# Kernel optimization log

Hardware: AMD Instinct MI355X
Metric: run time of the kernel (lower is better)

## Reference

```python
import jax, jax.numpy as jnp
import numpy as np

B, D_IN, T = 8, 1024, 2048
K, D_CB = 8192, 8
COMMIT = 0.005
CB_LOSS_W = 1.0
EPS = 1e-12  # F.normalize eps


def _wn(v, g):
    # torch weight_norm(dim=0) on a 1x1 Conv1d: w = g * v / ||v|| per output row
    return g[:, None] * v / jnp.linalg.norm(v, axis=1, keepdims=True)


def _l2n(x):
    return x / jnp.maximum(jnp.linalg.norm(x, axis=-1, keepdims=True), EPS)


def setup_inputs() -> dict:
    key = jax.random.key(0)
    ks = jax.random.split(key, 8)
    return {
        "z": jax.random.normal(ks[0], (B, D_IN, T), dtype=jnp.float32),
        "in_v": jax.random.normal(ks[1], (D_CB, D_IN), dtype=jnp.float32) * 0.02,
        "in_g": jnp.ones((D_CB,), dtype=jnp.float32),
        "in_b": jnp.zeros((D_CB,), dtype=jnp.float32),
        "out_v": jax.random.normal(ks[2], (D_IN, D_CB), dtype=jnp.float32) * 0.02,
        "out_g": jnp.ones((D_IN,), dtype=jnp.float32),
        "out_b": jnp.zeros((D_IN,), dtype=jnp.float32),
        "codebook": jax.random.normal(ks[3], (K, D_CB), dtype=jnp.float32),
    }


def reference(z, in_v, in_g, in_b, out_v, out_g, out_b, codebook):
    sg = jax.lax.stop_gradient
    # in_project: weight-normed 1x1 conv == matmul over channel dim
    w_in = _wn(in_v, in_g)
    z_e = jnp.einsum('oi,bit->bot', w_in, z) + in_b[None, :, None]  # [B, D_CB, T]

    # decode_latents
    enc = jnp.transpose(z_e, (0, 2, 1)).reshape(-1, D_CB)  # (B*T, D_CB)
    enc_n = _l2n(enc)
    cb_n = _l2n(codebook)
    dist = (jnp.sum(enc_n**2, axis=1, keepdims=True)
            - 2.0 * enc_n @ cb_n.T
            + jnp.sum(cb_n**2, axis=1)[None, :])  # (B*T, K)
    indices = jnp.argmin(dist, axis=1).reshape(B, T)  # [B, T]
    z_q = jnp.transpose(codebook[indices], (0, 2, 1))  # [B, D_CB, T] (unnormalized codebook)

    # training losses (per-batch means over (d, t))
    commit_loss = jnp.mean((z_e - sg(z_q)) ** 2, axis=(1, 2)) * COMMIT
    codebook_loss = jnp.mean((z_q - sg(z_e)) ** 2, axis=(1, 2)) * CB_LOSS_W

    # straight-through estimator
    z_q_st = z_e + sg(z_q - z_e)

    # out_project
    w_out = _wn(out_v, out_g)
    z_q_out = jnp.einsum('od,bdt->bot', w_out, z_q_st) + out_b[None, :, None]  # [B, D_IN, T]
    return (z_q_out, commit_loss, codebook_loss, indices, z_e)
```

## Files before the change

kernel.cpp:

```cpp
#include <hip/hip_runtime.h>
#include <math.h>
#include <stdint.h>

#define BB    8
#define DIN   1024
#define TT    2048
#define KK    8192
#define DCB   8
#define NPOS  (BB*TT)
#define KCHUNKS 64
#define KCH     (KK/KCHUNKS)
#define MARGIN  6e-4f

#define OFF_ZQOUT  0
#define OFF_COMMIT 16777216
#define OFF_CBLOSS 16777224
#define OFF_IDX    16777232
#define OFF_ZE     16793616

typedef short s8v __attribute__((ext_vector_type(8)));
typedef float f4v __attribute__((ext_vector_type(4)));

__device__ __forceinline__ unsigned short f2bf(float f) {
    unsigned u = __float_as_uint(f);
    u += 0x7FFF + ((u >> 16) & 1);
    return (unsigned short)(u >> 16);
}
__device__ __forceinline__ float bf2f(unsigned short h) {
    return __uint_as_float(((unsigned)h) << 16);
}

__global__ __launch_bounds__(256) void k_prep(
    const float* __restrict__ in_v, const float* __restrict__ in_g,
    const float* __restrict__ out_v, const float* __restrict__ out_g,
    const float* __restrict__ cb,
    float* __restrict__ w_in_f, float* __restrict__ w_out_f,
    double* __restrict__ cb_n, double* __restrict__ s_k,
    unsigned short* __restrict__ cb16, float* __restrict__ skp_f,
    double* __restrict__ lacc)
{
    __shared__ double red[256];
    int tid = threadIdx.x;
    int blk = blockIdx.x;

    if (blk < 8) {
        if (blk == 0 && tid < 64) lacc[tid] = 0.0;
        int r = blk;
        double s = 0.0;
        for (int i = tid; i < DIN; i += 256) {
            double v = (double)in_v[r*DIN + i];
            s += v*v;
        }
        red[tid] = s; __syncthreads();
        for (int off = 128; off > 0; off >>= 1) {
            if (tid < off) red[tid] += red[tid+off];
            __syncthreads();
        }
        double scale = (double)in_g[r] / sqrt(red[0]);
        for (int i = tid; i < DIN; i += 256)
            w_in_f[i*DCB + r] = (float)(scale * (double)in_v[r*DIN + i]);
    } else if (blk < 12) {
        int o = (blk-8)*256 + tid;
        float vv[DCB];
        double s = 0.0;
        #pragma unroll
        for (int d = 0; d < DCB; ++d) {
            vv[d] = out_v[o*DCB + d];
            s += (double)vv[d]*(double)vv[d];
        }
        double scale = (double)out_g[o] / sqrt(s);
        #pragma unroll
        for (int d = 0; d < DCB; ++d)
            w_out_f[o*DCB + d] = (float)(scale * (double)vv[d]);
    } else {
        int k = (blk-12)*256 + tid;
        double v[DCB]; double s = 0.0;
        #pragma unroll
        for (int d = 0; d < DCB; ++d) {
            v[d] = (double)cb[k*DCB + d];
            s += v[d]*v[d];
        }
        double nrm = sqrt(s);
        if (nrm < 1e-12) nrm = 1e-12;
        double s2 = 0.0;
        #pragma unroll
        for (int d = 0; d < DCB; ++d) {
            double t = v[d] / nrm;
            cb_n[(size_t)k*DCB + d] = t;
            s2 += t*t;
            float cf = (float)t;
            unsigned short bh = f2bf(cf);
            unsigned short bl = f2bf(cf - bf2f(bh));
            cb16[(size_t)k*16 + d]     = bh;
            cb16[(size_t)k*16 + 8 + d] = bl;
        }
        s_k[k] = s2;
        skp_f[k] = (float)(s2 + 4.0);
    }
}

__global__ __launch_bounds__(256) void k_inproj(
    const float* __restrict__ z, const float* __restrict__ w_in_f,
    const float* __restrict__ in_b,
    float* __restrict__ ze_out, double* __restrict__ enc_n,
    double* __restrict__ q_s, unsigned short* __restrict__ enc16)
{
    __shared__ float sm[DIN*DCB];

    int tid = threadIdx.x;
    {
        const uint4* src = (const uint4*)w_in_f;
        uint4* dst = (uint4*)sm;
        #pragma unroll
        for (int x = 0; x < 8; ++x) dst[tid + 256*x] = src[tid + 256*x];
    }
    __syncthreads();

    int p = tid & 7;
    int q = tid >> 3;
    int pos0 = blockIdx.x*32;
    int b = pos0 >> 11, t0 = pos0 & (TT-1);

    const float* zp = z + ((size_t)b*DIN + q)*TT + t0 + p*4;

    float acc[DCB][4];
    #pragma unroll
    for (int o = 0; o < DCB; ++o)
        #pragma unroll
        for (int j = 0; j < 4; ++j) acc[o][j] = 0.f;

    #pragma unroll
    for (int ii = 0; ii < 32; ++ii) {
        f4v zv = *(const f4v*)(zp + (size_t)ii*32*TT);
        const f4v* wp = (const f4v*)(sm + (ii*32 + q)*DCB);
        f4v w0 = wp[0], w1 = wp[1];
        #pragma unroll
        for (int j = 0; j < 4; ++j) {
            acc[0][j] += w0[0]*zv[j];
            acc[1][j] += w0[1]*zv[j];
            acc[2][j] += w0[2]*zv[j];
            acc[3][j] += w0[3]*zv[j];
            acc[4][j] += w1[0]*zv[j];
            acc[5][j] += w1[1]*zv[j];
            acc[6][j] += w1[2]*zv[j];
            acc[7][j] += w1[3]*zv[j];
        }
    }

    #pragma unroll
    for (int o = 0; o < DCB; ++o)
        #pragma unroll
        for (int j = 0; j < 4; ++j) {
            float v = acc[o][j];
            v += __shfl_xor(v, 8, 64);
            v += __shfl_xor(v, 16, 64);
            v += __shfl_xor(v, 32, 64);
            acc[o][j] = v;
        }

    __syncthreads();
    int lane = tid & 63, wv = tid >> 6;
    if ((lane >> 3) == 0) {
        float* rp = sm + wv*256 + p*32;
        #pragma unroll
        for (int o = 0; o < DCB; ++o)
            #pragma unroll
            for (int j = 0; j < 4; ++j) rp[o*4 + j] = acc[o][j];
    }
    __syncthreads();

    int o2 = tid & 7, p32 = tid >> 3;
    double s = 0.0;
    #pragma unroll
    for (int w2 = 0; w2 < 4; ++w2)
        s += (double)sm[w2*256 + (p32 >> 2)*32 + o2*4 + (p32 & 3)];
    s += (double)in_b[o2];

    int pos = pos0 + p32;
    int b3 = pos >> 11, t3 = pos & (TT-1);
    ze_out[((size_t)b3*DCB + o2)*TT + t3] = (float)s;

    double n2 = s*s;
    n2 += __shfl_xor(n2, 1, 64);
    n2 += __shfl_xor(n2, 2, 64);
    n2 += __shfl_xor(n2, 4, 64);
    double nrm = sqrt(n2);
    if (nrm < 1e-12) nrm = 1e-12;
    double e = s / nrm;
    enc_n[(size_t)pos*DCB + o2] = e;
    double s2 = e*e;
    s2 += __shfl_xor(s2, 1, 64);
    s2 += __shfl_xor(s2, 2, 64);
    s2 += __shfl_xor(s2, 4, 64);
    if (o2 == 0) q_s[pos] = s2;

    float ef = (float)(-2.0 * e);
    unsigned short ah = f2bf(ef);
    unsigned short al = f2bf(ef - bf2f(ah));
    enc16[(size_t)pos*16 + o2]     = ah;
    enc16[(size_t)pos*16 + 8 + o2] = al;
}

#define SCR_CB 8
__global__ __launch_bounds__(256) void k_screen(
    const unsigned short* __restrict__ enc16,
    const unsigned short* __restrict__ cb16,
    const float* __restrict__ skp_f,
    int* __restrict__ d1key)
{
    __shared__ unsigned short cbh[SCR_CB*KCH*8];
    __shared__ unsigned short cbl[SCR_CB*KCH*8];
    __shared__ float skl[SCR_CB*KCH];
    int tid = threadIdx.x;
    int cg = blockIdx.y;

    {
        const uint4* src = (const uint4*)(cb16 + (size_t)cg*SCR_CB*KCH*16);
        uint4* dh = (uint4*)cbh;
        uint4* dl = (uint4*)cbl;
        #pragma unroll
        for (int x = 0; x < 4; ++x) {
            int n = tid + 256*x;
            dh[n] = src[2*n];
            dl[n] = src[2*n + 1];
        }
        const float* ss = skp_f + (size_t)cg*SCR_CB*KCH;
        #pragma unroll
        for (int x = 0; x < 4; ++x) skl[tid + 256*x] = ss[tid + 256*x];
    }
    __syncthreads();

    int lane = tid & 63;
    int wv   = tid >> 6;
    int col  = lane & 15, quad = lane >> 4;
    int qbase = blockIdx.x*256 + wv*64;

    s8v bfr[4];
    #pragma unroll
    for (int f = 0; f < 4; ++f)
        bfr[f] = *(const s8v*)(enc16 + ((size_t)(qbase + f*16 + col))*16 + (quad >= 2 ? 8 : 0));

    const unsigned short* aplane = (quad & 1) ? cbl : cbh;

    for (int c2 = 0; c2 < SCR_CB; ++c2) {
        float dmin0 = INFINITY, dmin1 = INFINITY, dmin2 = INFINITY, dmin3 = INFINITY;
        #pragma unroll
        for (int t = 0; t < 8; ++t) {
            int nb = c2*KCH + t*16;
            s8v a = *(const s8v*)(aplane + (size_t)(nb + col)*8);
            f4v sk4 = *(const f4v*)(skl + nb + quad*4);
            f4v acc;
            acc = __builtin_amdgcn_mfma_f32_16x16x32_bf16(a, bfr[0], sk4, 0, 0, 0);
            dmin0 = fminf(dmin0, fminf(fminf(acc.x, acc.y), fminf(acc.z, acc.w)));
            acc = __builtin_amdgcn_mfma_f32_16x16x32_bf16(a, bfr[1], sk4, 0, 0, 0);
            dmin1 = fminf(dmin1, fminf(fminf(acc.x, acc.y), fminf(acc.z, acc.w)));
            acc = __builtin_amdgcn_mfma_f32_16x16x32_bf16(a, bfr[2], sk4, 0, 0, 0);
            dmin2 = fminf(dmin2, fminf(fminf(acc.x, acc.y), fminf(acc.z, acc.w)));
            acc = __builtin_amdgcn_mfma_f32_16x16x32_bf16(a, bfr[3], sk4, 0, 0, 0);
            dmin3 = fminf(dmin3, fminf(fminf(acc.x, acc.y), fminf(acc.z, acc.w)));
        }
        int chunk = cg*SCR_CB + c2;
        float dm[4] = {dmin0, dmin1, dmin2, dmin3};
        #pragma unroll
        for (int f = 0; f < 4; ++f) {
            float v = dm[f];
            v = fminf(v, __shfl_xor(v, 16, 64));
            v = fminf(v, __shfl_xor(v, 32, 64));
            if (quad == 0)
                d1key[(size_t)(qbase + f*16 + col)*KCHUNKS + chunk] = __float_as_int(v);
        }
    }
}

__global__ __launch_bounds__(256) void k_verify(
    const int* __restrict__ d1key,
    const double* __restrict__ enc_n, const double* __restrict__ q_s,
    const double* __restrict__ cb_n, const double* __restrict__ s_k,
    const float* __restrict__ cb, const float* __restrict__ ze,
    float* __restrict__ idx_f, int* __restrict__ idx_i,
    double* __restrict__ lacc)
{
    __shared__ double sred[4];
    int tid = threadIdx.x;
    int lane = tid & 63;
    int wv = tid >> 6;
    int pos = blockIdx.x*4 + wv;

    int myk = d1key[(size_t)pos*KCHUNKS + lane];
    int m = myk;
    #pragma unroll
    for (int off = 1; off < 64; off <<= 1) m = min(m, __shfl_xor(m, off, 64));
    float thr = __int_as_float(m & 0xFFFFFF80) + MARGIN;
    bool scan = __int_as_float(myk & 0xFFFFFF80) <= thr;
    unsigned long long mask = __ballot(scan);

    double e[DCB];
    #pragma unroll
    for (int d = 0; d < DCB; ++d) e[d] = enc_n[(size_t)pos*DCB + d];
    double qs = q_s[pos];

    double bd = 1e300; int bi = 0x7FFFFFFF;
    while (mask) {
        int c = __ffsll((long long)mask) - 1;
        mask &= mask - 1;
        #pragma unroll
        for (int r = 0; r < KCH/64; ++r) {
            int k = c*KCH + r*64 + lane;
            const double* cp = cb_n + (size_t)k*DCB;
            double dot = e[0]*cp[0] + e[1]*cp[1] + e[2]*cp[2] + e[3]*cp[3]
                       + e[4]*cp[4] + e[5]*cp[5] + e[6]*cp[6] + e[7]*cp[7];
            double dist = qs - 2.0*dot + s_k[k];
            if (dist < bd || (dist == bd && k < bi)) { bd = dist; bi = k; }
        }
    }
    #pragma unroll
    for (int off = 1; off < 64; off <<= 1) {
        double od = __shfl_xor(bd, off, 64);
        int    oi = __shfl_xor(bi, off, 64);
        if (od < bd || (od == bd && oi < bi)) { bd = od; bi = oi; }
    }
    if (lane == 0) {
        int b = pos >> 11, t = pos & (TT-1);
        idx_f[pos] = (float)bi;
        idx_i[pos] = bi;
        double ssum = 0.0;
        #pragma unroll
        for (int d = 0; d < DCB; ++d) {
            double zev = (double)ze[((size_t)b*DCB + d)*TT + t];
            double zqv = (double)cb[bi*DCB + d];
            double diff = zev - zqv;
            ssum += diff*diff;
        }
        sred[wv] = ssum;
    }
    __syncthreads();
    if (tid == 0) {
        double t4 = sred[0] + sred[1] + sred[2] + sred[3];
        int b = (blockIdx.x*4) >> 11;
        atomicAdd(&lacc[b*8 + (blockIdx.x & 7)], t4);
    }
}

__global__ __launch_bounds__(256) void k_out_proj(
    const float* __restrict__ cb, const float* __restrict__ ze,
    const int* __restrict__ idx_i, const float* __restrict__ w_out,
    const float* __restrict__ out_b, const double* __restrict__ lacc,
    float* __restrict__ commit_out, float* __restrict__ cbloss_out,
    float* __restrict__ zq_out)
{
    __shared__ float wl[128*DCB];
    __shared__ float bl[128];
    int tid = threadIdx.x;

    if (blockIdx.x == 0 && blockIdx.y == 0 && tid < 8) {
        double s = 0.0;
        #pragma unroll
        for (int j = 0; j < 8; ++j) s += lacc[tid*8 + j];
        double mm = s / (double)(DCB*TT);
        commit_out[tid] = (float)(mm * 0.005);
        cbloss_out[tid] = (float)mm;
    }

    int oc = blockIdx.y;
    int obase = oc*128;
    for (int x = tid; x < 128*DCB; x += 256) wl[x] = w_out[obase*DCB + x];
    for (int x = tid; x < 128; x += 256) bl[x] = out_b[obase + x];
    __syncthreads();

    int pos = blockIdx.x*256 + tid;
    int b = pos >> 11, t = pos & (TT-1);
    int ki = idx_i[pos];
    float zq[DCB];
    #pragma unroll
    for (int d = 0; d < DCB; ++d) {
        float zev = ze[((size_t)b*DCB + d)*TT + t];
        float zqv = cb[ki*DCB + d];
        zq[d] = zev + (zqv - zev);
    }
    float* outp = zq_out + ((size_t)b*DIN + obase)*TT + t;
    for (int oo = 0; oo < 128; ++oo) {
        float acc = 0.f;
        #pragma unroll
        for (int d = 0; d < DCB; ++d) acc += wl[oo*DCB + d]*zq[d];
        acc += bl[oo];
        outp[(size_t)oo*TT] = acc;
    }
}

extern "C" void kernel_launch(void* const* d_in, const int* in_sizes, int n_in,
                              void* d_out, int out_size, void* d_ws, size_t ws_size,
                              hipStream_t stream)
{
    const float* z        = (const float*)d_in[0];
    const float* in_v     = (const float*)d_in[1];
    const float* in_g     = (const float*)d_in[2];
    const float* in_b     = (const float*)d_in[3];
    const float* out_v    = (const float*)d_in[4];
    const float* out_g    = (const float*)d_in[5];
    const float* out_b    = (const float*)d_in[6];
    const float* codebook = (const float*)d_in[7];

    float* out = (float*)d_out;
    float* zq_out_p  = out + OFF_ZQOUT;
    float* commit_p  = out + OFF_COMMIT;
    float* cbloss_p  = out + OFF_CBLOSS;
    float* idx_p     = out + OFF_IDX;
    float* ze_p      = out + OFF_ZE;

    float*  w_in_f = (float*)d_ws;
    double* cb_n   = (double*)d_ws + DCB*DIN;
    double* s_k    = cb_n + (size_t)KK*DCB;
    double* enc_n  = s_k + KK;
    double* q_s    = enc_n + (size_t)NPOS*DCB;
    double* loss_q = q_s + NPOS;
    float*  w_out  = (float*)(loss_q + NPOS);
    float*  skp_f  = w_out + DCB*DIN;
    unsigned short* cb16  = (unsigned short*)(skp_f + KK);
    unsigned short* enc16 = cb16 + (size_t)KK*16;
    int*    d1key  = (int*)(enc16 + (size_t)NPOS*16);
    int*    idx_i  = d1key + (size_t)NPOS*KCHUNKS;
    double* lacc   = (double*)(idx_i + NPOS);

    k_prep<<<44, 256, 0, stream>>>(in_v, in_g, out_v, out_g, codebook,
                                   w_in_f, w_out, cb_n, s_k, cb16, skp_f, lacc);
    k_inproj<<<NPOS/32, 256, 0, stream>>>(z, w_in_f, in_b, ze_p, enc_n, q_s, enc16);
    k_screen<<<dim3(NPOS/256, KCHUNKS/SCR_CB), 256, 0, stream>>>(
        enc16, cb16, skp_f, d1key);
    k_verify<<<NPOS/4, 256, 0, stream>>>(d1key, enc_n, q_s, cb_n, s_k,
                                         codebook, ze_p, idx_p, idx_i, lacc);
    k_out_proj<<<dim3(NPOS/256, DIN/128), 256, 0, stream>>>(
        codebook, ze_p, idx_i, w_out, out_b, lacc, commit_p, cbloss_p, zq_out_p);
}
```

Baseline: 180.0 us.

## Vectorize out-projection stores with 4 positions per thread and nontemporal I/O

The out-projection kernel now has each thread handle 4 consecutive time positions for 32 output channels instead of 1 position for 128 channels. It reads ze, indices and codebook rows as float4/int4 and writes float4 results with nontemporal stores. The in-projection streaming load of z also uses a nontemporal load, and the codebook normalization multiplies by a reciprocal instead of dividing. The aim is wider memory transactions and less cache pollution on the large 64MB output write and the z read. In exchange, each thread holds more registers.

```diff
diff --git a/kernel.cpp b/kernel.cpp
--- a/kernel.cpp
+++ b/kernel.cpp
@@ -82,10 +82,11 @@
         }
         double nrm = sqrt(s);
         if (nrm < 1e-12) nrm = 1e-12;
+        double rinv = 1.0 / nrm;
         double s2 = 0.0;
         #pragma unroll
         for (int d = 0; d < DCB; ++d) {
-            double t = v[d] / nrm;
+            double t = v[d] * rinv;
             cb_n[(size_t)k*DCB + d] = t;
             s2 += t*t;
             float cf = (float)t;
@@ -131,7 +132,7 @@
 
     #pragma unroll
     for (int ii = 0; ii < 32; ++ii) {
-        f4v zv = *(const f4v*)(zp + (size_t)ii*32*TT);
+        f4v zv = __builtin_nontemporal_load((const f4v*)(zp + (size_t)ii*32*TT));
         const f4v* wp = (const f4v*)(sm + (ii*32 + q)*DCB);
         f4v w0 = wp[0], w1 = wp[1];
         #pragma unroll
@@ -364,26 +365,52 @@
     int oc = blockIdx.y;
     int obase = oc*128;
     for (int x = tid; x < 128*DCB; x += 256) wl[x] = w_out[obase*DCB + x];
-    for (int x = tid; x < 128; x += 256) bl[x] = out_b[obase + x];
-    __syncthreads();
-
-    int pos = blockIdx.x*256 + tid;
-    int b = pos >> 11, t = pos & (TT-1);
-    int ki = idx_i[pos];
-    float zq[DCB];
+    if (tid < 128) bl[tid] = out_b[obase + tid];
+    __syncthreads();
+
+    int tq = tid & 63;
+    int og = tid >> 6;
+    int pos0 = blockIdx.x*256;
+    int b = pos0 >> 11;
+    int t0 = (pos0 & (TT-1)) + tq*4;
+    int posq = pos0 + tq*4;
+
+    int4 ki4 = *(const int4*)(idx_i + posq);
+    int kiA[4] = {ki4.x, ki4.y, ki4.z, ki4.w};
+
+    float zq[4][DCB];
     #pragma unroll
     for (int d = 0; d < DCB; ++d) {
-        float zev = ze[((size_t)b*DCB + d)*TT + t];
-        float zqv = cb[ki*DCB + d];
-        zq[d] = zev + (zqv - zev);
-    }
-    float* outp = zq_out + ((size_t)b*DIN + obase)*TT + t;
-    for (int oo = 0; oo < 128; ++oo) {
-        float acc = 0.f;
-        #pragma unroll
-        for (int d = 0; d < DCB; ++d) acc += wl[oo*DCB + d]*zq[d];
-        acc += bl[oo];
-        outp[(size_t)oo*TT] = acc;
+        f4v ze4 = *(const f4v*)(ze + ((size_t)b*DCB + d)*TT + t0);
+        #pragma unroll
+        for (int j = 0; j < 4; ++j) zq[j][d] = ze4[j];
+    }
+    #pragma unroll
+    for (int j = 0; j < 4; ++j) {
+        f4v c0 = *(const f4v*)(cb + (size_t)kiA[j]*DCB);
+        f4v c1 = *(const f4v*)(cb + (size_t)kiA[j]*DCB + 4);
+        #pragma unroll
+        for (int d = 0; d < 4; ++d) {
+            zq[j][d]   = zq[j][d]   + (c0[d] - zq[j][d]);
+            zq[j][d+4] = zq[j][d+4] + (c1[d] - zq[j][d+4]);
+        }
+    }
+
+    const f4v* wv4 = (const f4v*)wl;
+    float* outp = zq_out + ((size_t)b*DIN + obase + og*32)*TT + t0;
+    #pragma unroll 4
+    for (int oi = 0; oi < 32; ++oi) {
+        int oo = og*32 + oi;
+        f4v w0 = wv4[oo*2], w1 = wv4[oo*2+1];
+        float bo = bl[oo];
+        f4v accv;
+        #pragma unroll
+        for (int j = 0; j < 4; ++j) {
+            float acc = w0[0]*zq[j][0] + w0[1]*zq[j][1] + w0[2]*zq[j][2] + w0[3]*zq[j][3]
+                      + w1[0]*zq[j][4] + w1[1]*zq[j][5] + w1[2]*zq[j][6] + w1[3]*zq[j][7];
+            accv[j] = acc + bo;
+        }
+        __builtin_nontemporal_store(accv, (f4v*)(outp + (size_t)oi*TT));
     }
 }
 
```

Measured after the change: 185.0 us. 1.03x slower.
